# Optimization experiments

Hardware: AMD Instinct MI355X
Metric: run time of the kernel (lower is better)

## Reference

```python
import jax, jax.numpy as jnp
import numpy as np

NEG_SLOPE = 0.2


def gatv2_conv(h, src, dst, W, attn, n_nodes, residual=False, W_res=None, activation=None):
    """DGL GATv2Conv with share_weights=True, bias=False, no dropout (eval).

    h: [N, F_in]; W: [F_in, H*D]; attn: [H, D]; src/dst: [E] edge endpoints.
    Returns [N, H, D].
    """
    H, D = attn.shape
    feat = (h @ W).reshape(n_nodes, H, D)              # shared src/dst projection
    # GATv2 scoring: e_ij = a^T LeakyReLU(W h_i + W h_j)
    e = jax.nn.leaky_relu(feat[src] + feat[dst], NEG_SLOPE)   # [E, H, D]
    logits = jnp.einsum('ehd,hd->eh', e, attn)                 # [E, H]
    # edge softmax over incoming edges of each dst node
    m = jax.ops.segment_max(logits, dst, num_segments=n_nodes)  # [N, H]
    ex = jnp.exp(logits - jax.lax.stop_gradient(m)[dst])
    denom = jax.ops.segment_sum(ex, dst, num_segments=n_nodes)  # [N, H]
    a = ex / denom[dst]                                          # [E, H]
    # aggregate: sum_j a_ij * (W h_j)
    rst = jax.ops.segment_sum(a[:, :, None] * feat[src], dst, num_segments=n_nodes)  # [N, H, D]
    if residual:
        res = h @ W_res if W_res is not None else h
        rst = rst + res.reshape(n_nodes, H, D)
    if activation is not None:
        rst = activation(rst)
    return rst


def setup_inputs() -> dict:
    key = jax.random.key(0)
    ks = jax.random.split(key, 12)
    N, E, F_IN, D, H, C, HO = 50000, 500000, 128, 32, 4, 40, 6
    inputs = jax.random.normal(ks[0], (N, F_IN), dtype=jnp.float32)
    src = jax.random.randint(ks[1], (E,), 0, N)
    dst = jax.random.randint(ks[2], (E,), 0, N)
    def glorot(k, shape):
        fan = shape[0]
        return jax.random.normal(k, shape, dtype=jnp.float32) / np.sqrt(fan)
    W0 = glorot(ks[3], (F_IN, H * D))
    attn0 = glorot(ks[4], (H, D))
    W1 = glorot(ks[5], (H * D, H * D))
    attn1 = glorot(ks[6], (H, D))
    W2 = glorot(ks[7], (H * D, HO * C))
    attn2 = glorot(ks[8], (HO, C))
    Wres2 = glorot(ks[9], (H * D, HO * C))
    return {"inputs": inputs, "src": src, "dst": dst, "W0": W0, "attn0": attn0,
            "W1": W1, "attn1": attn1, "W2": W2, "attn2": attn2, "Wres2": Wres2}


def reference(inputs, src, dst, W0, attn0, W1, attn1, W2, attn2, Wres2):
    N = inputs.shape[0]
    act = jax.nn.elu
    # layer 0: no residual, elu, flatten heads
    h = gatv2_conv(inputs, src, dst, W0, attn0, N, residual=False, activation=act)
    h = h.reshape(N, -1)
    # layer 1: identity residual (in == heads*out), elu, flatten heads
    h = gatv2_conv(h, src, dst, W1, attn1, N, residual=True, W_res=None, activation=act)
    h = h.reshape(N, -1)
    # output layer: linear residual, no activation, mean over heads
    out = gatv2_conv(h, src, dst, W2, attn2, N, residual=True, W_res=Wres2, activation=None)
    return out.mean(axis=1)  # [N, num_classes]
```

## Files before the change

kernel.cpp:

```cpp
#include <hip/hip_runtime.h>
#include <math.h>


#define LRELU(x) ((x) >= 0.f ? (x) : 0.2f * (x))

__global__ void k_zero(int* __restrict__ cnt, int* __restrict__ fill, int N) {
  int i = blockIdx.x * blockDim.x + threadIdx.x;
  if (i < N) { cnt[i] = 0; fill[i] = 0; }
}

__global__ void k_count(const int* __restrict__ dst, int* __restrict__ cnt, int E) {
  int e = blockIdx.x * blockDim.x + threadIdx.x;
  if (e < E) atomicAdd(&cnt[dst[e]], 1);
}

__global__ void k_scan1(const int* __restrict__ cnt, int* __restrict__ row_ptr,
                        int* __restrict__ bsum, int N) {
  __shared__ int s[256];
  int tid = threadIdx.x;
  int i = blockIdx.x * 256 + tid;
  int v = (i < N) ? cnt[i] : 0;
  s[tid] = v;
  __syncthreads();
  for (int off = 1; off < 256; off <<= 1) {
    int t = (tid >= off) ? s[tid - off] : 0;
    __syncthreads();
    s[tid] += t;
    __syncthreads();
  }
  if (i < N) row_ptr[i] = s[tid] - v;
  if (tid == 255) bsum[blockIdx.x] = s[255];
}

__global__ void k_scan2(int* __restrict__ bsum, int nb) {
  __shared__ int s[256];
  int t = threadIdx.x;
  int v = (t < nb) ? bsum[t] : 0;
  s[t] = v;
  __syncthreads();
  for (int off = 1; off < 256; off <<= 1) {
    int tt = (t >= off) ? s[t - off] : 0;
    __syncthreads();
    s[t] += tt;
    __syncthreads();
  }
  if (t < nb) bsum[t] = s[t] - v;
}

__global__ void k_scan3(int* __restrict__ row_ptr, const int* __restrict__ bsum, int N, int E) {
  int i = blockIdx.x * blockDim.x + threadIdx.x;
  if (i < N) row_ptr[i] += bsum[i >> 8];
  else if (i == N) row_ptr[N] = E;
}

__global__ void k_scatter(const int* __restrict__ src, const int* __restrict__ dst,
                          const int* __restrict__ row_ptr, int* __restrict__ fill,
                          int* __restrict__ csr_src, int E) {
  int e = blockIdx.x * blockDim.x + threadIdx.x;
  if (e >= E) return;
  int d = dst[e];
  int pos = row_ptr[d] + atomicAdd(&fill[d], 1);
  csr_src[pos] = src[e];
}

__global__ void k_wmean(const float* __restrict__ wres2, float* __restrict__ wm) {
  int i = blockIdx.x * blockDim.x + threadIdx.x;
  if (i >= 128 * 40) return;
  int k = i / 40, c = i % 40;
  float s = 0.f;
#pragma unroll
  for (int ho = 0; ho < 6; ++ho) s += wres2[k * 240 + ho * 40 + c];
  wm[i] = s * (1.0f / 6.0f);
}

template <int LDC>
__global__ __launch_bounds__(256) void k_gemm(const float* __restrict__ A,
                                              const float* __restrict__ B,
                                              float* __restrict__ C, int N) {
  __shared__ __align__(16) float As[16][64];
  __shared__ __align__(16) float Bs[16][128];
  const int tid = threadIdx.x;
  const int row0 = blockIdx.x * 64;
  const int col_base = (blockIdx.y == 0) ? 0 : (LDC - 128);
  const int ty = tid >> 4, tx = tid & 15;
  const int r0 = ty * 4;
  const int arow = tid & 63;
  const int akc = (tid >> 6) * 4;
  int gra = row0 + arow;
  if (gra >= N) gra = N - 1;
  const float* Ap = A + (size_t)gra * 128 + akc;
  const int f0 = tid * 4, f1 = f0 + 1024;
  const int b0r = f0 >> 7, b0c = f0 & 127;
  const int b1r = f1 >> 7, b1c = f1 & 127;

  float acc[4][8] = {};

#pragma unroll 1
  for (int kk = 0; kk < 128; kk += 16) {
    __syncthreads();
    float4 av = *(const float4*)(Ap + kk);
    float4 bv0 = *(const float4*)&B[(size_t)(kk + b0r) * LDC + col_base + b0c];
    float4 bv1 = *(const float4*)&B[(size_t)(kk + b1r) * LDC + col_base + b1c];
    As[akc + 0][arow] = av.x;
    As[akc + 1][arow] = av.y;
    As[akc + 2][arow] = av.z;
    As[akc + 3][arow] = av.w;
    *(float4*)&Bs[b0r][b0c] = bv0;
    *(float4*)&Bs[b1r][b1c] = bv1;
    __syncthreads();
#pragma unroll
    for (int k = 0; k < 16; ++k) {
      float a[4], b[8];
      *(float4*)&a[0] = *(const float4*)&As[k][r0];
      *(float4*)&b[0] = *(const float4*)&Bs[k][tx * 4];
      *(float4*)&b[4] = *(const float4*)&Bs[k][64 + tx * 4];
#pragma unroll
      for (int i = 0; i < 4; ++i)
#pragma unroll
        for (int j = 0; j < 8; ++j) acc[i][j] += a[i] * b[j];
    }
  }

  const int gc_lo = col_base + tx * 4;
  const int gc_hi = col_base + 64 + tx * 4;
  const bool lo_ok = (blockIdx.y == 0) || (gc_lo >= 128);
#pragma unroll
  for (int i = 0; i < 4; ++i) {
    int gr = row0 + r0 + i;
    if (gr < N) {
      if (lo_ok) *(float4*)&C[(size_t)gr * LDC + gc_lo] = *(float4*)&acc[i][0];
      *(float4*)&C[(size_t)gr * LDC + gc_hi] = *(float4*)&acc[i][4];
    }
  }
}

__global__ __launch_bounds__(256) void k_resmean(const float* __restrict__ A,
                                                 const float* __restrict__ Wm,
                                                 float* __restrict__ out, int N) {
  __shared__ float w[128 * 40];
  for (int i = threadIdx.x; i < 128 * 40; i += 256) w[i] = Wm[i];
  __syncthreads();
  int r = blockIdx.x * 256 + threadIdx.x;
  if (r >= N) return;
  float acc[40] = {};
  for (int k = 0; k < 128; k += 4) {
    float4 hv = *(const float4*)&A[(size_t)r * 128 + k];
#pragma unroll
    for (int j = 0; j < 40; ++j)
      acc[j] += hv.x * w[(k + 0) * 40 + j] + hv.y * w[(k + 1) * 40 + j] +
                hv.z * w[(k + 2) * 40 + j] + hv.w * w[(k + 3) * 40 + j];
  }
#pragma unroll
  for (int j = 0; j < 40; j += 4)
    *(float4*)&out[(size_t)r * 40 + j] = make_float4(acc[j], acc[j + 1], acc[j + 2], acc[j + 3]);
}

template <bool RES>
__global__ __launch_bounds__(256) void k_agg_fused(const float* __restrict__ feat,
                                                   const float* __restrict__ attn,
                                                   const int* __restrict__ row_ptr,
                                                   const int* __restrict__ csr_src,
                                                   const float* __restrict__ hres,
                                                   float* __restrict__ out, int N) {
  int wid = (blockIdx.x * 256 + threadIdx.x) >> 6;
  bool nok = wid < N;
  int n = nok ? wid : (N - 1);
  int lane = threadIdx.x & 63;
  int half = lane >> 5;
  int c = (lane & 31) * 4;
  float4 fd = *(const float4*)&feat[(size_t)n * 128 + c];
  float4 av = *(const float4*)&attn[c];
  int p0 = row_ptr[n], p1 = row_ptr[n + 1];
  float m = -1e30f, s = 0.f;
  float4 acc = {0.f, 0.f, 0.f, 0.f};
  for (int p = p0; p < p1; p += 2) {
    int pp = p + half;
    bool v = pp < p1;
    int si = csr_src[v ? pp : p];
    float4 fs = *(const float4*)&feat[(size_t)si * 128 + c];
    float x0 = LRELU(fs.x + fd.x), x1 = LRELU(fs.y + fd.y);
    float x2 = LRELU(fs.z + fd.z), x3 = LRELU(fs.w + fd.w);
    float x = av.x * x0 + av.y * x1 + av.z * x2 + av.w * x3;
    x += __shfl_xor(x, 1);
    x += __shfl_xor(x, 2);
    x += __shfl_xor(x, 4);
    float mn = fmaxf(m, x);
    float sc = __expf(m - mn);
    float pe = v ? __expf(x - mn) : 0.f;
    s = s * sc + pe;
    acc.x = acc.x * sc + pe * fs.x;
    acc.y = acc.y * sc + pe * fs.y;
    acc.z = acc.z * sc + pe * fs.z;
    acc.w = acc.w * sc + pe * fs.w;
    m = mn;
  }
  float m2 = __shfl_xor(m, 32);
  float s2 = __shfl_xor(s, 32);
  float4 a2;
  a2.x = __shfl_xor(acc.x, 32);
  a2.y = __shfl_xor(acc.y, 32);
  a2.z = __shfl_xor(acc.z, 32);
  a2.w = __shfl_xor(acc.w, 32);
  float mT = fmaxf(m, m2);
  float f1 = __expf(m - mT), f2 = __expf(m2 - mT);
  float ssum = s * f1 + s2 * f2;
  float inv = (p1 > p0) ? 1.0f / ssum : 0.f;
  float4 r;
  r.x = (acc.x * f1 + a2.x * f2) * inv;
  r.y = (acc.y * f1 + a2.y * f2) * inv;
  r.z = (acc.z * f1 + a2.z * f2) * inv;
  r.w = (acc.w * f1 + a2.w * f2) * inv;
  if (RES) {
    float4 hv = *(const float4*)&hres[(size_t)n * 128 + c];
    r.x += hv.x; r.y += hv.y; r.z += hv.z; r.w += hv.w;
  }
  r.x = r.x > 0.f ? r.x : expm1f(r.x);
  r.y = r.y > 0.f ? r.y : expm1f(r.y);
  r.z = r.z > 0.f ? r.z : expm1f(r.z);
  r.w = r.w > 0.f ? r.w : expm1f(r.w);
  if (half == 0 && nok) *(float4*)&out[(size_t)n * 128 + c] = r;
}

__global__ __launch_bounds__(256) void k_agg2_fused(const float* __restrict__ feat2,
                                                    const float* __restrict__ attn2,
                                                    const int* __restrict__ row_ptr,
                                                    const int* __restrict__ csr_src,
                                                    const float* __restrict__ resm,
                                                    float* __restrict__ out, int N) {
  __shared__ float rs[4][240];
  int w = threadIdx.x >> 6;
  int wid = blockIdx.x * 4 + w;
  bool nok = wid < N;
  int n = nok ? wid : (N - 1);
  int lane = threadIdx.x & 63;
  bool act = lane < 60;
  int ho = lane / 10, t = lane % 10;
  int g0 = ho * 10;
  int fo = act ? (ho * 40 + t * 4) : 0;
  float4 zero = {0.f, 0.f, 0.f, 0.f};
  float4 fd = act ? *(const float4*)&feat2[(size_t)n * 240 + fo] : zero;
  float4 av = act ? *(const float4*)&attn2[fo] : zero;
  int p0 = row_ptr[n], p1 = row_ptr[n + 1];
  float mA = -1e30f, sA = 0.f, mB = -1e30f, sB = 0.f;
  float4 aA = zero, aB = zero;
  for (int p = p0; p < p1; p += 2) {
    int iA = csr_src[p];
    bool vB = (p + 1) < p1;
    int iB = vB ? csr_src[p + 1] : iA;
    float4 fA = *(const float4*)&feat2[(size_t)iA * 240 + fo];
    float4 fB = *(const float4*)&feat2[(size_t)iB * 240 + fo];
    float xA = av.x * LRELU(fA.x + fd.x) + av.y * LRELU(fA.y + fd.y) +
               av.z * LRELU(fA.z + fd.z) + av.w * LRELU(fA.w + fd.w);
    float xB = av.x * LRELU(fB.x + fd.x) + av.y * LRELU(fB.y + fd.y) +
               av.z * LRELU(fB.z + fd.z) + av.w * LRELU(fB.w + fd.w);
    float aAx = xA + __shfl(xA, lane + 5);
    float aBx = xB + __shfl(xB, lane + 5);
    float bAx = aAx + __shfl(aAx, lane + 1);
    float bBx = aBx + __shfl(aBx, lane + 1);
    float cAx = bAx + __shfl(bAx, lane + 2);
    float cBx = bBx + __shfl(bBx, lane + 2);
    float SA = cAx + __shfl(aAx, lane + 4);
    float SB = cBx + __shfl(aBx, lane + 4);
    float lA = __shfl(SA, g0);
    float lB = __shfl(SB, g0);
    float mnA = fmaxf(mA, lA);
    float scA = __expf(mA - mnA);
    float peA = __expf(lA - mnA);
    sA = sA * scA + peA;
    aA.x = aA.x * scA + peA * fA.x;
    aA.y = aA.y * scA + peA * fA.y;
    aA.z = aA.z * scA + peA * fA.z;
    aA.w = aA.w * scA + peA * fA.w;
    mA = mnA;
    float mnB = fmaxf(mB, lB);
    float scB = __expf(mB - mnB);
    float peB = vB ? __expf(lB - mnB) : 0.f;
    sB = sB * scB + peB;
    aB.x = aB.x * scB + peB * fB.x;
    aB.y = aB.y * scB + peB * fB.y;
    aB.z = aB.z * scB + peB * fB.z;
    aB.w = aB.w * scB + peB * fB.w;
    mB = mnB;
  }
  float mT = fmaxf(mA, mB);
  float f1 = __expf(mA - mT), f2 = __expf(mB - mT);
  float ssum = sA * f1 + sB * f2;
  float inv = (p1 > p0) ? 1.0f / ssum : 0.f;
  float4 r;
  r.x = (aA.x * f1 + aB.x * f2) * inv;
  r.y = (aA.y * f1 + aB.y * f2) * inv;
  r.z = (aA.z * f1 + aB.z * f2) * inv;
  r.w = (aA.w * f1 + aB.w * f2) * inv;
  if (act) *(float4*)&rs[w][fo] = r;
  __syncthreads();
  if (lane < 10 && nok) {
#pragma unroll
    for (int k = 0; k < 4; ++k) {
      int cc = t * 4 + k;
      float v = (rs[w][cc] + rs[w][40 + cc] + rs[w][80 + cc] + rs[w][120 + cc] +
                 rs[w][160 + cc] + rs[w][200 + cc]) * (1.0f / 6.0f) +
                resm[(size_t)n * 40 + cc];
      out[(size_t)n * 40 + cc] = v;
    }
  }
}

extern "C" void kernel_launch(void* const* d_in, const int* in_sizes, int n_in,
                              void* d_out, int out_size, void* d_ws, size_t ws_size,
                              hipStream_t stream) {
  const float* inputs = (const float*)d_in[0];
  const int* src = (const int*)d_in[1];
  const int* dst = (const int*)d_in[2];
  const float* W0 = (const float*)d_in[3];
  const float* attn0 = (const float*)d_in[4];
  const float* W1 = (const float*)d_in[5];
  const float* attn1 = (const float*)d_in[6];
  const float* W2 = (const float*)d_in[7];
  const float* attn2 = (const float*)d_in[8];
  const float* Wres2 = (const float*)d_in[9];
  const int N = in_sizes[0] / 128;
  const int E = in_sizes[1];

  char* base = (char*)d_ws;
  size_t off = 0;
  auto alloc = [&](size_t bytes) -> void* {
    void* q = base + off;
    off += (bytes + 255) & ~(size_t)255;
    return q;
  };
  int* cnt = (int*)alloc((size_t)N * 4);
  int* fill = (int*)alloc((size_t)N * 4);
  int* row_ptr = (int*)alloc((size_t)(N + 1) * 4);
  int* bsum = (int*)alloc(1024 * 4);
  int* csr_src = (int*)alloc((size_t)E * 4);
  float* F = (float*)alloc((size_t)N * 240 * 4);
  float* h1 = (float*)alloc((size_t)N * 128 * 4);
  float* h2 = (float*)alloc((size_t)N * 128 * 4);
  float* resm = (float*)alloc((size_t)N * 40 * 4);
  float* wm = (float*)alloc(128 * 40 * 4);
  (void)ws_size;

  const int nb1 = (N + 255) / 256;
  const int nrb = (N + 63) / 64;

  hipLaunchKernelGGL(k_zero, dim3((N + 255) / 256), dim3(256), 0, stream, cnt, fill, N);
  hipLaunchKernelGGL(k_count, dim3((E + 255) / 256), dim3(256), 0, stream, dst, cnt, E);
  hipLaunchKernelGGL(k_scan1, dim3(nb1), dim3(256), 0, stream, cnt, row_ptr, bsum, N);
  hipLaunchKernelGGL(k_scan2, dim3(1), dim3(256), 0, stream, bsum, nb1);
  hipLaunchKernelGGL(k_scan3, dim3((N + 256) / 256), dim3(256), 0, stream, row_ptr, bsum, N, E);
  hipLaunchKernelGGL(k_scatter, dim3((E + 255) / 256), dim3(256), 0, stream, src, dst, row_ptr,
                     fill, csr_src, E);
  hipLaunchKernelGGL(k_wmean, dim3((128 * 40 + 255) / 256), dim3(256), 0, stream, Wres2, wm);

  hipLaunchKernelGGL((k_gemm<128>), dim3(nrb, 1), dim3(256), 0, stream, inputs, W0, F, N);
  hipLaunchKernelGGL((k_agg_fused<false>), dim3((N + 3) / 4), dim3(256), 0, stream, F, attn0,
                     row_ptr, csr_src, (const float*)nullptr, h1, N);
  hipLaunchKernelGGL((k_gemm<128>), dim3(nrb, 1), dim3(256), 0, stream, h1, W1, F, N);
  hipLaunchKernelGGL((k_agg_fused<true>), dim3((N + 3) / 4), dim3(256), 0, stream, F, attn1,
                     row_ptr, csr_src, h1, h2, N);
  hipLaunchKernelGGL((k_gemm<240>), dim3(nrb, 2), dim3(256), 0, stream, h2, W2, F, N);
  hipLaunchKernelGGL(k_resmean, dim3((N + 255) / 256), dim3(256), 0, stream, h2, wm, resm, N);
  hipLaunchKernelGGL(k_agg2_fused, dim3((N + 3) / 4), dim3(256), 0, stream, F, attn2, row_ptr,
                     csr_src, resm, (float*)d_out, N);
}
```

Measured before the change: 478.6 us.

## Double-buffer GEMM shared tiles and widen edge loops for more in-flight gathers

```diff
diff --git a/kernel.cpp b/kernel.cpp
--- a/kernel.cpp
+++ b/kernel.cpp
@@ -3,6 +3,18 @@
 
 
 #define LRELU(x) ((x) >= 0.f ? (x) : 0.2f * (x))
+
+#define MERGE4(mA, sA, aA, mB, sB, aB)                          \
+  {                                                             \
+    float mT_ = fmaxf(mA, mB);                                  \
+    float f1_ = __expf((mA) - mT_), f2_ = __expf((mB) - mT_);   \
+    sA = (sA)*f1_ + (sB)*f2_;                                   \
+    aA.x = aA.x * f1_ + aB.x * f2_;                             \
+    aA.y = aA.y * f1_ + aB.y * f2_;                             \
+    aA.z = aA.z * f1_ + aB.z * f2_;                             \
+    aA.w = aA.w * f1_ + aB.w * f2_;                             \
+    mA = mT_;                                                   \
+  }
 
 __global__ void k_zero(int* __restrict__ cnt, int* __restrict__ fill, int N) {
   int i = blockIdx.x * blockDim.x + threadIdx.x;
@@ -77,8 +89,8 @@
 __global__ __launch_bounds__(256) void k_gemm(const float* __restrict__ A,
                                               const float* __restrict__ B,
                                               float* __restrict__ C, int N) {
-  __shared__ __align__(16) float As[16][64];
-  __shared__ __align__(16) float Bs[16][128];
+  __shared__ __align__(16) float As[2][16][64];
+  __shared__ __align__(16) float Bs[2][16][128];
   const int tid = threadIdx.x;
   const int row0 = blockIdx.x * 64;
   const int col_base = (blockIdx.y == 0) ? 0 : (LDC - 128);
@@ -95,29 +107,45 @@
 
   float acc[4][8] = {};
 
+  float4 av = *(const float4*)(Ap + 0);
+  float4 bv0 = *(const float4*)&B[(size_t)b0r * LDC + col_base + b0c];
+  float4 bv1 = *(const float4*)&B[(size_t)b1r * LDC + col_base + b1c];
+  As[0][akc + 0][arow] = av.x;
+  As[0][akc + 1][arow] = av.y;
+  As[0][akc + 2][arow] = av.z;
+  As[0][akc + 3][arow] = av.w;
+  *(float4*)&Bs[0][b0r][b0c] = bv0;
+  *(float4*)&Bs[0][b1r][b1c] = bv1;
+
 #pragma unroll 1
-  for (int kk = 0; kk < 128; kk += 16) {
+  for (int i = 0; i < 8; ++i) {
     __syncthreads();
-    float4 av = *(const float4*)(Ap + kk);
-    float4 bv0 = *(const float4*)&B[(size_t)(kk + b0r) * LDC + col_base + b0c];
-    float4 bv1 = *(const float4*)&B[(size_t)(kk + b1r) * LDC + col_base + b1c];
-    As[akc + 0][arow] = av.x;
-    As[akc + 1][arow] = av.y;
-    As[akc + 2][arow] = av.z;
-    As[akc + 3][arow] = av.w;
-    *(float4*)&Bs[b0r][b0c] = bv0;
-    *(float4*)&Bs[b1r][b1c] = bv1;
-    __syncthreads();
+    const int buf = i & 1;
+    if (i < 7) {
+      const int kk = (i + 1) * 16;
+      av = *(const float4*)(Ap + kk);
+      bv0 = *(const float4*)&B[(size_t)(kk + b0r) * LDC + col_base + b0c];
+      bv1 = *(const float4*)&B[(size_t)(kk + b1r) * LDC + col_base + b1c];
+    }
 #pragma unroll
     for (int k = 0; k < 16; ++k) {
       float a[4], b[8];
-      *(float4*)&a[0] = *(const float4*)&As[k][r0];
-      *(float4*)&b[0] = *(const float4*)&Bs[k][tx * 4];
-      *(float4*)&b[4] = *(const float4*)&Bs[k][64 + tx * 4];
-#pragma unroll
-      for (int i = 0; i < 4; ++i)
-#pragma unroll
-        for (int j = 0; j < 8; ++j) acc[i][j] += a[i] * b[j];
+      *(float4*)&a[0] = *(const float4*)&As[buf][k][r0];
+      *(float4*)&b[0] = *(const float4*)&Bs[buf][k][tx * 4];
+      *(float4*)&b[4] = *(const float4*)&Bs[buf][k][64 + tx * 4];
+#pragma unroll
+      for (int ii = 0; ii < 4; ++ii)
+#pragma unroll
+        for (int jj = 0; jj < 8; ++jj) acc[ii][jj] += a[ii] * b[jj];
+    }
+    if (i < 7) {
+      const int nb = buf ^ 1;
+      As[nb][akc + 0][arow] = av.x;
+      As[nb][akc + 1][arow] = av.y;
+      As[nb][akc + 2][arow] = av.z;
+      As[nb][akc + 3][arow] = av.w;
+      *(float4*)&Bs[nb][b0r][b0c] = bv0;
+      *(float4*)&Bs[nb][b1r][b1c] = bv1;
     }
   }
 
@@ -171,45 +199,63 @@
   float4 fd = *(const float4*)&feat[(size_t)n * 128 + c];
   float4 av = *(const float4*)&attn[c];
   int p0 = row_ptr[n], p1 = row_ptr[n + 1];
-  float m = -1e30f, s = 0.f;
-  float4 acc = {0.f, 0.f, 0.f, 0.f};
-  for (int p = p0; p < p1; p += 2) {
-    int pp = p + half;
-    bool v = pp < p1;
-    int si = csr_src[v ? pp : p];
-    float4 fs = *(const float4*)&feat[(size_t)si * 128 + c];
-    float x0 = LRELU(fs.x + fd.x), x1 = LRELU(fs.y + fd.y);
-    float x2 = LRELU(fs.z + fd.z), x3 = LRELU(fs.w + fd.w);
-    float x = av.x * x0 + av.y * x1 + av.z * x2 + av.w * x3;
-    x += __shfl_xor(x, 1);
-    x += __shfl_xor(x, 2);
-    x += __shfl_xor(x, 4);
-    float mn = fmaxf(m, x);
-    float sc = __expf(m - mn);
-    float pe = v ? __expf(x - mn) : 0.f;
-    s = s * sc + pe;
-    acc.x = acc.x * sc + pe * fs.x;
-    acc.y = acc.y * sc + pe * fs.y;
-    acc.z = acc.z * sc + pe * fs.z;
-    acc.w = acc.w * sc + pe * fs.w;
-    m = mn;
-  }
-  float m2 = __shfl_xor(m, 32);
-  float s2 = __shfl_xor(s, 32);
+  float4 zero = {0.f, 0.f, 0.f, 0.f};
+  float mA = -1e30f, sA = 0.f, mB = -1e30f, sB = 0.f;
+  float4 aA = zero, aB = zero;
+  for (int p = p0; p < p1; p += 4) {
+    int pA = p + half;
+    int pB = p + 2 + half;
+    bool vA = pA < p1, vB = pB < p1;
+    int iA = csr_src[vA ? pA : p0];
+    int iB = csr_src[vB ? pB : p0];
+    float4 fA = *(const float4*)&feat[(size_t)iA * 128 + c];
+    float4 fB = *(const float4*)&feat[(size_t)iB * 128 + c];
+    float xA = av.x * LRELU(fA.x + fd.x) + av.y * LRELU(fA.y + fd.y) +
+               av.z * LRELU(fA.z + fd.z) + av.w * LRELU(fA.w + fd.w);
+    float xB = av.x * LRELU(fB.x + fd.x) + av.y * LRELU(fB.y + fd.y) +
+               av.z * LRELU(fB.z + fd.z) + av.w * LRELU(fB.w + fd.w);
+    xA += __shfl_xor(xA, 1);
+    xB += __shfl_xor(xB, 1);
+    xA += __shfl_xor(xA, 2);
+    xB += __shfl_xor(xB, 2);
+    xA += __shfl_xor(xA, 4);
+    xB += __shfl_xor(xB, 4);
+    float mnA = fmaxf(mA, xA);
+    float scA = __expf(mA - mnA);
+    float peA = vA ? __expf(xA - mnA) : 0.f;
+    sA = sA * scA + peA;
+    aA.x = aA.x * scA + peA * fA.x;
+    aA.y = aA.y * scA + peA * fA.y;
+    aA.z = aA.z * scA + peA * fA.z;
+    aA.w = aA.w * scA + peA * fA.w;
+    mA = mnA;
+    float mnB = fmaxf(mB, xB);
+    float scB = __expf(mB - mnB);
+    float peB = vB ? __expf(xB - mnB) : 0.f;
+    sB = sB * scB + peB;
+    aB.x = aB.x * scB + peB * fB.x;
+    aB.y = aB.y * scB + peB * fB.y;
+    aB.z = aB.z * scB + peB * fB.z;
+    aB.w = aB.w * scB + peB * fB.w;
+    mB = mnB;
+  }
+  MERGE4(mA, sA, aA, mB, sB, aB);
+  float m2 = __shfl_xor(mA, 32);
+  float s2 = __shfl_xor(sA, 32);
   float4 a2;
-  a2.x = __shfl_xor(acc.x, 32);
-  a2.y = __shfl_xor(acc.y, 32);
-  a2.z = __shfl_xor(acc.z, 32);
-  a2.w = __shfl_xor(acc.w, 32);
-  float mT = fmaxf(m, m2);
-  float f1 = __expf(m - mT), f2 = __expf(m2 - mT);
-  float ssum = s * f1 + s2 * f2;
+  a2.x = __shfl_xor(aA.x, 32);
+  a2.y = __shfl_xor(aA.y, 32);
+  a2.z = __shfl_xor(aA.z, 32);
+  a2.w = __shfl_xor(aA.w, 32);
+  float mT = fmaxf(mA, m2);
+  float f1 = __expf(mA - mT), f2 = __expf(m2 - mT);
+  float ssum = sA * f1 + s2 * f2;
   float inv = (p1 > p0) ? 1.0f / ssum : 0.f;
   float4 r;
-  r.x = (acc.x * f1 + a2.x * f2) * inv;
-  r.y = (acc.y * f1 + a2.y * f2) * inv;
-  r.z = (acc.z * f1 + a2.z * f2) * inv;
-  r.w = (acc.w * f1 + a2.w * f2) * inv;
+  r.x = (aA.x * f1 + a2.x * f2) * inv;
+  r.y = (aA.y * f1 + a2.y * f2) * inv;
+  r.z = (aA.z * f1 + a2.z * f2) * inv;
+  r.w = (aA.w * f1 + a2.w * f2) * inv;
   if (RES) {
     float4 hv = *(const float4*)&hres[(size_t)n * 128 + c];
     r.x += hv.x; r.y += hv.y; r.z += hv.z; r.w += hv.w;
@@ -241,56 +287,58 @@
   float4 fd = act ? *(const float4*)&feat2[(size_t)n * 240 + fo] : zero;
   float4 av = act ? *(const float4*)&attn2[fo] : zero;
   int p0 = row_ptr[n], p1 = row_ptr[n + 1];
-  float mA = -1e30f, sA = 0.f, mB = -1e30f, sB = 0.f;
-  float4 aA = zero, aB = zero;
-  for (int p = p0; p < p1; p += 2) {
-    int iA = csr_src[p];
-    bool vB = (p + 1) < p1;
-    int iB = vB ? csr_src[p + 1] : iA;
-    float4 fA = *(const float4*)&feat2[(size_t)iA * 240 + fo];
-    float4 fB = *(const float4*)&feat2[(size_t)iB * 240 + fo];
-    float xA = av.x * LRELU(fA.x + fd.x) + av.y * LRELU(fA.y + fd.y) +
-               av.z * LRELU(fA.z + fd.z) + av.w * LRELU(fA.w + fd.w);
-    float xB = av.x * LRELU(fB.x + fd.x) + av.y * LRELU(fB.y + fd.y) +
-               av.z * LRELU(fB.z + fd.z) + av.w * LRELU(fB.w + fd.w);
-    float aAx = xA + __shfl(xA, lane + 5);
-    float aBx = xB + __shfl(xB, lane + 5);
-    float bAx = aAx + __shfl(aAx, lane + 1);
-    float bBx = aBx + __shfl(aBx, lane + 1);
-    float cAx = bAx + __shfl(bAx, lane + 2);
-    float cBx = bBx + __shfl(bBx, lane + 2);
-    float SA = cAx + __shfl(aAx, lane + 4);
-    float SB = cBx + __shfl(aBx, lane + 4);
-    float lA = __shfl(SA, g0);
-    float lB = __shfl(SB, g0);
-    float mnA = fmaxf(mA, lA);
-    float scA = __expf(mA - mnA);
-    float peA = __expf(lA - mnA);
-    sA = sA * scA + peA;
-    aA.x = aA.x * scA + peA * fA.x;
-    aA.y = aA.y * scA + peA * fA.y;
-    aA.z = aA.z * scA + peA * fA.z;
-    aA.w = aA.w * scA + peA * fA.w;
-    mA = mnA;
-    float mnB = fmaxf(mB, lB);
-    float scB = __expf(mB - mnB);
-    float peB = vB ? __expf(lB - mnB) : 0.f;
-    sB = sB * scB + peB;
-    aB.x = aB.x * scB + peB * fB.x;
-    aB.y = aB.y * scB + peB * fB.y;
-    aB.z = aB.z * scB + peB * fB.z;
-    aB.w = aB.w * scB + peB * fB.w;
-    mB = mnB;
-  }
-  float mT = fmaxf(mA, mB);
-  float f1 = __expf(mA - mT), f2 = __expf(mB - mT);
-  float ssum = sA * f1 + sB * f2;
-  float inv = (p1 > p0) ? 1.0f / ssum : 0.f;
+  float m_[4], s_[4];
+  float4 a_[4];
+#pragma unroll
+  for (int j = 0; j < 4; ++j) { m_[j] = -1e30f; s_[j] = 0.f; a_[j] = zero; }
+  for (int p = p0; p < p1; p += 4) {
+    int idx[4];
+    bool val[4];
+#pragma unroll
+    for (int j = 0; j < 4; ++j) {
+      int pp = p + j;
+      val[j] = pp < p1;
+      idx[j] = csr_src[val[j] ? pp : p];
+    }
+    float4 f_[4];
+#pragma unroll
+    for (int j = 0; j < 4; ++j) f_[j] = *(const float4*)&feat2[(size_t)idx[j] * 240 + fo];
+    float x_[4], aa_[4], S_[4];
+#pragma unroll
+    for (int j = 0; j < 4; ++j)
+      x_[j] = av.x * LRELU(f_[j].x + fd.x) + av.y * LRELU(f_[j].y + fd.y) +
+              av.z * LRELU(f_[j].z + fd.z) + av.w * LRELU(f_[j].w + fd.w);
+#pragma unroll
+    for (int j = 0; j < 4; ++j) aa_[j] = x_[j] + __shfl(x_[j], lane + 5);
+#pragma unroll
+    for (int j = 0; j < 4; ++j) S_[j] = aa_[j] + __shfl(aa_[j], lane + 1);
+#pragma unroll
+    for (int j = 0; j < 4; ++j) S_[j] = S_[j] + __shfl(S_[j], lane + 2);
+#pragma unroll
+    for (int j = 0; j < 4; ++j) S_[j] = S_[j] + __shfl(aa_[j], lane + 4);
+#pragma unroll
+    for (int j = 0; j < 4; ++j) {
+      float l = __shfl(S_[j], g0);
+      float mn = fmaxf(m_[j], l);
+      float sc = __expf(m_[j] - mn);
+      float pe = val[j] ? __expf(l - mn) : 0.f;
+      s_[j] = s_[j] * sc + pe;
+      a_[j].x = a_[j].x * sc + pe * f_[j].x;
+      a_[j].y = a_[j].y * sc + pe * f_[j].y;
+      a_[j].z = a_[j].z * sc + pe * f_[j].z;
+      a_[j].w = a_[j].w * sc + pe * f_[j].w;
+      m_[j] = mn;
+    }
+  }
+  MERGE4(m_[0], s_[0], a_[0], m_[1], s_[1], a_[1]);
+  MERGE4(m_[2], s_[2], a_[2], m_[3], s_[3], a_[3]);
+  MERGE4(m_[0], s_[0], a_[0], m_[2], s_[2], a_[2]);
+  float inv = (p1 > p0) ? 1.0f / s_[0] : 0.f;
   float4 r;
-  r.x = (aA.x * f1 + aB.x * f2) * inv;
-  r.y = (aA.y * f1 + aB.y * f2) * inv;
-  r.z = (aA.z * f1 + aB.z * f2) * inv;
-  r.w = (aA.w * f1 + aB.w * f2) * inv;
+  r.x = a_[0].x * inv;
+  r.y = a_[0].y * inv;
+  r.z = a_[0].z * inv;
+  r.w = a_[0].w * inv;
   if (act) *(float4*)&rs[w][fo] = r;
   __syncthreads();
   if (lane < 10 && nok) {
```

Result: faster. 466.6 us (-2.5%).
